# Performance work log

Hardware: AMD Instinct MI355X
Metric: run time of the kernel (lower is better)

## Reference

```python
import jax, jax.numpy as jnp
import numpy as np

N = 50000
IN_F = 512
HID = 64
HEADS = 4
CLASSES = 6
E = 800000
NEG_SLOPE = 0.2


def setup_inputs() -> dict:
    key = jax.random.key(0)
    ks = jax.random.split(key, 12)
    s = 1.0 / np.sqrt(IN_F)
    s2 = 1.0 / np.sqrt(HID * HEADS)
    return {
        "x": jax.random.normal(ks[0], (N, IN_F), dtype=jnp.float32),
        "edge_index": jax.random.randint(ks[1], (2, E), 0, N, dtype=jnp.int32),
        "W1": jax.random.normal(ks[2], (IN_F, HEADS * HID), dtype=jnp.float32) * s,
        "a_src1": jax.random.normal(ks[3], (HEADS, HID), dtype=jnp.float32) * s,
        "a_dst1": jax.random.normal(ks[4], (HEADS, HID), dtype=jnp.float32) * s,
        "b1": jnp.zeros((HEADS * HID,), dtype=jnp.float32),
        "W2": jax.random.normal(ks[5], (HEADS * HID, CLASSES), dtype=jnp.float32) * s2,
        "a_src2": jax.random.normal(ks[6], (1, CLASSES), dtype=jnp.float32) * s2,
        "a_dst2": jax.random.normal(ks[7], (1, CLASSES), dtype=jnp.float32) * s2,
        "b2": jnp.zeros((CLASSES,), dtype=jnp.float32),
    }


def gat_conv(x, src, dst, W, a_src, a_dst, bias, heads, ch):
    # x: [N, F] -> h: [N, H, C]
    n = x.shape[0]
    h = (x @ W).reshape(n, heads, ch)
    # per-node attention halves: [N, H]
    e_src = jnp.einsum('nhc,hc->nh', h, a_src)
    e_dst = jnp.einsum('nhc,hc->nh', h, a_dst)
    # per-edge logits with leaky relu: [E', H]
    logits = jax.nn.leaky_relu(e_src[src] + e_dst[dst], NEG_SLOPE)
    # segment softmax over incoming edges of each dst node
    m = jax.ops.segment_max(logits, dst, num_segments=n)  # [N, H]
    p = jnp.exp(logits - m[dst])
    denom = jax.ops.segment_sum(p, dst, num_segments=n)   # [N, H] (>0: self loops)
    alpha = p / denom[dst]                                 # [E', H]
    # weighted scatter-aggregate: [N, H, C]
    out = jax.ops.segment_sum(alpha[:, :, None] * h[src], dst, num_segments=n)
    return out.reshape(n, heads * ch) + bias


def reference(x, edge_index, W1, a_src1, a_dst1, b1, W2, a_src2, a_dst2, b2):
    n = x.shape[0]
    loops = jnp.arange(n, dtype=edge_index.dtype)
    src = jnp.concatenate([edge_index[0], loops])  # PyG add_self_loops
    dst = jnp.concatenate([edge_index[1], loops])
    h = gat_conv(x, src, dst, W1, a_src1, a_dst1, b1, HEADS, HID)
    h = jax.nn.elu(h)
    out = gat_conv(h, src, dst, W2, a_src2, a_dst2, b2, 1, CLASSES)
    return jax.nn.log_softmax(out, axis=1)
```

## Files before the change

### kernel.cpp

```cpp
#include <hip/hip_runtime.h>

#define HEADS 4
#define HID 64
#define CH1 256
#define CLS 6
#define H2S 8
#define NSLOPE 0.2f

typedef short bf16x8 __attribute__((ext_vector_type(8)));
typedef float f32x4 __attribute__((ext_vector_type(4)));

__device__ __forceinline__ float leaky(float x) {
  return (x >= 0.f) ? x : NSLOPE * x;
}

__device__ __forceinline__ ushort f2bf(float f) {
  unsigned u = __float_as_uint(f);
  unsigned r = (u + 0x7FFFu + ((u >> 16) & 1u)) >> 16;
  return (ushort)r;
}

__device__ __forceinline__ float bf2f(ushort u) {
  return __uint_as_float((unsigned)u << 16);
}

__global__ void k_count_cvt(const int* __restrict__ ei, int E, int Etot,
                            int* __restrict__ cnt, int eb,
                            const float* __restrict__ W1, ushort* __restrict__ w1t) {
  int b = blockIdx.x;
  if (b < eb) {
    int e = b * 256 + threadIdx.x;
    if (e >= Etot) return;
    int d = (e < E) ? ei[E + e] : e - E;
    atomicAdd(&cnt[d], 1);
  } else {
    int t = (b - eb) * 256 + threadIdx.x;
    if (t >= 512 * 256) return;
    int k = t >> 8, c = t & 255;
    w1t[c * 512 + k] = f2bf(W1[t]);
  }
}

__global__ __launch_bounds__(256) void k_gemm1_mfma(
    const float* __restrict__ x,
    const ushort* __restrict__ w1t,
    const float* __restrict__ a_src, const float* __restrict__ a_dst,
    ushort* __restrict__ h1b, float* __restrict__ es, float* __restrict__ ed,
    int M) {
  __shared__ ushort ldsA[2][2048];
  int t = threadIdx.x;
  int wid = t >> 6, lane = t & 63;
  int brow = blockIdx.x * 64;

  int rA = t >> 2, qA = t & 3, lsA = qA ^ (rA & 3);
  int rowA = brow + rA; if (rowA >= M) rowA = M - 1;
  const float* srcA = x + (size_t)rowA * 512 + lsA * 8;
  int dAw = t * 8;

  int l15 = lane & 15, g = lane >> 4;
  int sw = ((g ^ (lane & 3)) << 3);
  int aoff[4];
#pragma unroll
  for (int m = 0; m < 4; ++m) aoff[m] = (m * 16 + l15) * 32 + sw;

  const ushort* bp[4];
#pragma unroll
  for (int n = 0; n < 4; ++n)
    bp[n] = w1t + (size_t)(wid * 64 + n * 16 + l15) * 512 + g * 8;

  f32x4 acc[4][4] = {};
  f32x4 aLo, aHi;

#define LOADA(kt) do { \
    aLo = *(const f32x4*)(srcA + (kt) * 32); \
    aHi = *(const f32x4*)(srcA + (kt) * 32 + 4); \
  } while (0)

#define WRITEA(buf) do { \
    union { unsigned u[4]; bf16x8 b; } cv; \
    asm("v_cvt_pk_bf16_f32 %0, %1, %2" : "=v"(cv.u[0]) : "v"(aLo[0]), "v"(aLo[1])); \
    asm("v_cvt_pk_bf16_f32 %0, %1, %2" : "=v"(cv.u[1]) : "v"(aLo[2]), "v"(aLo[3])); \
    asm("v_cvt_pk_bf16_f32 %0, %1, %2" : "=v"(cv.u[2]) : "v"(aHi[0]), "v"(aHi[1])); \
    asm("v_cvt_pk_bf16_f32 %0, %1, %2" : "=v"(cv.u[3]) : "v"(aHi[2]), "v"(aHi[3])); \
    *(bf16x8*)&ldsA[buf][dAw] = cv.b; \
  } while (0)

  bf16x8 bv[2][4];
#pragma unroll
  for (int n = 0; n < 4; ++n) bv[0][n] = *(const bf16x8*)bp[n];
  LOADA(0);
  WRITEA(0);
  __syncthreads();

#pragma unroll
  for (int kt = 0; kt < 16; ++kt) {
    const int cur = kt & 1;
    if (kt < 15) {
      LOADA(kt + 1);
#pragma unroll
      for (int n = 0; n < 4; ++n)
        bv[(kt + 1) & 1][n] = *(const bf16x8*)(bp[n] + (kt + 1) * 32);
    }
    bf16x8 av[4];
#pragma unroll
    for (int m = 0; m < 4; ++m) av[m] = *(const bf16x8*)&ldsA[cur][aoff[m]];
#pragma unroll
    for (int m = 0; m < 4; ++m)
#pragma unroll
      for (int n = 0; n < 4; ++n)
        acc[m][n] = __builtin_amdgcn_mfma_f32_16x16x32_bf16(av[m], bv[cur][n], acc[m][n], 0, 0, 0);
    if (kt < 15) WRITEA(cur ^ 1);
    __syncthreads();
  }
#undef LOADA
#undef WRITEA

  float as4[4], ad4[4];
#pragma unroll
  for (int n = 0; n < 4; ++n) {
    int c = wid * 64 + n * 16 + l15;
    as4[n] = a_src[c];
    ad4[n] = a_dst[c];
  }
  int rbase = g * 4;
#pragma unroll
  for (int m = 0; m < 4; ++m) {
#pragma unroll
    for (int r = 0; r < 4; ++r) {
      int grow = brow + m * 16 + rbase + r;
      bool ok = grow < M;
      float ps = 0.f, pd = 0.f;
#pragma unroll
      for (int n = 0; n < 4; ++n) {
        float v = acc[m][n][r];
        ps += v * as4[n];
        pd += v * ad4[n];
        if (ok) h1b[(size_t)grow * CH1 + wid * 64 + n * 16 + l15] = f2bf(v);
      }
#pragma unroll
      for (int o = 1; o < 16; o <<= 1) {
        ps += __shfl_xor(ps, o);
        pd += __shfl_xor(pd, o);
      }
      if (l15 == 0 && ok) {
        es[grow * HEADS + wid] = ps;
        ed[grow * HEADS + wid] = pd;
      }
    }
  }
}

__global__ __launch_bounds__(256) void k_scan1(int* __restrict__ deg,
    int* __restrict__ rowptr, int* __restrict__ bsum, int n) {
  int i = blockIdx.x * 256 + threadIdx.x;
  int v = (i < n) ? deg[i] : 0;
  if (i < n) deg[i] = 0;
  int lane = threadIdx.x & 63, wave = threadIdx.x >> 6;
  int incl = v;
#pragma unroll
  for (int o = 1; o < 64; o <<= 1) {
    int u = __shfl_up(incl, o);
    if (lane >= o) incl += u;
  }
  __shared__ int ws4[4];
  if (lane == 63) ws4[wave] = incl;
  __syncthreads();
  if (threadIdx.x == 0) {
    int run = 0;
    for (int w = 0; w < 4; ++w) { int x = ws4[w]; ws4[w] = run; run += x; }
    bsum[blockIdx.x] = run;
  }
  __syncthreads();
  if (i < n) rowptr[i] = incl - v + ws4[wave];
}

__global__ __launch_bounds__(256) void k_scan3(int* __restrict__ rowptr,
    const int* __restrict__ bsum, int n, int Etot, int nb) {
  int t = threadIdx.x;
  int b = blockIdx.x;
  int v = (t < b && t < nb) ? bsum[t] : 0;
  int lane = t & 63, wave = t >> 6;
#pragma unroll
  for (int o = 32; o; o >>= 1) v += __shfl_xor(v, o);
  __shared__ int ws4[4];
  if (lane == 0) ws4[wave] = v;
  __syncthreads();
  int base = ws4[0] + ws4[1] + ws4[2] + ws4[3];
  int i = b * 256 + t;
  if (i < n) rowptr[i] += base;
  if (i == 0) rowptr[n] = Etot;
}

__global__ void k_scatter(const int* __restrict__ ei, int E, int Etot,
    const int* __restrict__ rowptr, int* __restrict__ cursor,
    int* __restrict__ esrc) {
  int e = blockIdx.x * blockDim.x + threadIdx.x;
  if (e >= Etot) return;
  int s, d;
  if (e < E) { s = ei[e]; d = ei[E + e]; } else { s = d = e - E; }
  int pos = rowptr[d] + atomicAdd(&cursor[d], 1);
  esrc[pos] = s;
}

__global__ __launch_bounds__(256) void k_agg1_csr(const int* __restrict__ rowptr,
    const int* __restrict__ esrc, const float* __restrict__ es,
    const float* __restrict__ ed, const ushort* __restrict__ h1b,
    const float* __restrict__ b1, const float* __restrict__ W2,
    const float* __restrict__ a_src2, const float* __restrict__ a_dst2,
    float* __restrict__ h2, float* __restrict__ es2, float* __restrict__ ed2,
    int Nn) {
  __shared__ int   spi[4][64];
  __shared__ float spp[4][64 * 4];
  int wid = threadIdx.x >> 6, lane = threadIdx.x & 63;
  int ch = lane * 4;
  float w2s[4][CLS];
#pragma unroll
  for (int c = 0; c < 4; ++c)
#pragma unroll
    for (int j = 0; j < CLS; ++j)
      w2s[c][j] = W2[(ch + c) * CLS + j];

  int d = blockIdx.x * 4 + wid;
  if (d >= Nn) return;
  int beg = rowptr[d], end = rowptr[d + 1];
  float4 edv = *(const float4*)&ed[d * 4];
  int myhead = lane >> 4;
  const char* hcb = (const char*)h1b + (size_t)ch * 2;

  float4 acc = make_float4(0.f, 0.f, 0.f, 0.f);
  float4 den4 = make_float4(0.f, 0.f, 0.f, 0.f);
  const float* pp = &spp[wid][0];
  for (int c0 = beg; c0 < end; c0 += 64) {
    int i = c0 + lane;
    int s = 0;
    float4 p = make_float4(0.f, 0.f, 0.f, 0.f);
    if (i < end) {
      s = esrc[i];
      float4 e4 = *(const float4*)&es[s * 4];
      p.x = __expf(leaky(e4.x + edv.x));
      p.y = __expf(leaky(e4.y + edv.y));
      p.z = __expf(leaky(e4.z + edv.z));
      p.w = __expf(leaky(e4.w + edv.w));
    }
    den4.x += p.x; den4.y += p.y; den4.z += p.z; den4.w += p.w;
    spi[wid][lane] = s << 9;
    *(float4*)&spp[wid][lane * 4] = p;
    int cl = min(64, end - c0);
    int j = 0;
    for (; j + 3 < cl; j += 4) {
      int o0 = spi[wid][j],     o1 = spi[wid][j + 1];
      int o2 = spi[wid][j + 2], o3 = spi[wid][j + 3];
      float p0 = pp[j * 4 + myhead],       p1 = pp[(j + 1) * 4 + myhead];
      float p2 = pp[(j + 2) * 4 + myhead], p3 = pp[(j + 3) * 4 + myhead];
      ushort4 v0 = *(const ushort4*)(hcb + o0);
      ushort4 v1 = *(const ushort4*)(hcb + o1);
      ushort4 v2 = *(const ushort4*)(hcb + o2);
      ushort4 v3 = *(const ushort4*)(hcb + o3);
      acc.x += p0 * bf2f(v0.x) + p1 * bf2f(v1.x) + p2 * bf2f(v2.x) + p3 * bf2f(v3.x);
      acc.y += p0 * bf2f(v0.y) + p1 * bf2f(v1.y) + p2 * bf2f(v2.y) + p3 * bf2f(v3.y);
      acc.z += p0 * bf2f(v0.z) + p1 * bf2f(v1.z) + p2 * bf2f(v2.z) + p3 * bf2f(v3.z);
      acc.w += p0 * bf2f(v0.w) + p1 * bf2f(v1.w) + p2 * bf2f(v2.w) + p3 * bf2f(v3.w);
    }
    for (; j < cl; ++j) {
      int oj = spi[wid][j];
      float pj = pp[j * 4 + myhead];
      ushort4 v = *(const ushort4*)(hcb + oj);
      acc.x += pj * bf2f(v.x);
      acc.y += pj * bf2f(v.y);
      acc.z += pj * bf2f(v.z);
      acc.w += pj * bf2f(v.w);
    }
  }
#pragma unroll
  for (int o = 32; o; o >>= 1) {
    den4.x += __shfl_xor(den4.x, o);
    den4.y += __shfl_xor(den4.y, o);
    den4.z += __shfl_xor(den4.z, o);
    den4.w += __shfl_xor(den4.w, o);
  }
  float den = (myhead == 0) ? den4.x : (myhead == 1) ? den4.y
            : (myhead == 2) ? den4.z : den4.w;
  float4 b4 = *(const float4*)&b1[ch];
  float4 r;
  r.x = acc.x / den + b4.x; r.x = (r.x > 0.f) ? r.x : expm1f(r.x);
  r.y = acc.y / den + b4.y; r.y = (r.y > 0.f) ? r.y : expm1f(r.y);
  r.z = acc.z / den + b4.z; r.z = (r.z > 0.f) ? r.z : expm1f(r.z);
  r.w = acc.w / den + b4.w; r.w = (r.w > 0.f) ? r.w : expm1f(r.w);

  float q0 = r.x * w2s[0][0] + r.y * w2s[1][0] + r.z * w2s[2][0] + r.w * w2s[3][0];
  float q1 = r.x * w2s[0][1] + r.y * w2s[1][1] + r.z * w2s[2][1] + r.w * w2s[3][1];
  float q2 = r.x * w2s[0][2] + r.y * w2s[1][2] + r.z * w2s[2][2] + r.w * w2s[3][2];
  float q3 = r.x * w2s[0][3] + r.y * w2s[1][3] + r.z * w2s[2][3] + r.w * w2s[3][3];
  float q4 = r.x * w2s[0][4] + r.y * w2s[1][4] + r.z * w2s[2][4] + r.w * w2s[3][4];
  float q5 = r.x * w2s[0][5] + r.y * w2s[1][5] + r.z * w2s[2][5] + r.w * w2s[3][5];
#pragma unroll
  for (int o = 32; o; o >>= 1) {
    q0 += __shfl_xor(q0, o); q1 += __shfl_xor(q1, o); q2 += __shfl_xor(q2, o);
    q3 += __shfl_xor(q3, o); q4 += __shfl_xor(q4, o); q5 += __shfl_xor(q5, o);
  }
  if (lane == 0) {
    float* h2r = &h2[(size_t)d * H2S];
    h2r[0] = q0; h2r[1] = q1; h2r[2] = q2; h2r[3] = q3; h2r[4] = q4; h2r[5] = q5;
    es2[d] = q0 * a_src2[0] + q1 * a_src2[1] + q2 * a_src2[2]
           + q3 * a_src2[3] + q4 * a_src2[4] + q5 * a_src2[5];
    ed2[d] = q0 * a_dst2[0] + q1 * a_dst2[1] + q2 * a_dst2[2]
           + q3 * a_dst2[3] + q4 * a_dst2[4] + q5 * a_dst2[5];
  }
}

__global__ __launch_bounds__(256) void k_l2(const int* __restrict__ rowptr,
    const int* __restrict__ esrc, const float* __restrict__ es2,
    const float* __restrict__ ed2, const float* __restrict__ h2,
    const float* __restrict__ b2, float* __restrict__ out, int Nn) {
  int t = threadIdx.x;
  int grp = t >> 3, sl = t & 7;
  int n = blockIdx.x * 32 + grp;
  if (n >= Nn) return;
  int beg = rowptr[n], end = rowptr[n + 1];
  float edv = ed2[n];
  float den = 0.f, a0 = 0.f, a1 = 0.f, a2 = 0.f, a3 = 0.f, a4 = 0.f, a5 = 0.f;
  for (int i = beg + sl; i < end; i += 8) {
    int s = esrc[i];
    float p = __expf(leaky(es2[s] + edv));
    den += p;
    const float* hr = &h2[(size_t)s * H2S];
    float4 v0 = *(const float4*)hr;
    float2 v1 = *(const float2*)(hr + 4);
    a0 += p * v0.x; a1 += p * v0.y; a2 += p * v0.z;
    a3 += p * v0.w; a4 += p * v1.x; a5 += p * v1.y;
  }
#pragma unroll
  for (int o = 1; o < 8; o <<= 1) {
    den += __shfl_xor(den, o);
    a0 += __shfl_xor(a0, o); a1 += __shfl_xor(a1, o); a2 += __shfl_xor(a2, o);
    a3 += __shfl_xor(a3, o); a4 += __shfl_xor(a4, o); a5 += __shfl_xor(a5, o);
  }
  if (sl == 0) {
    float v[CLS];
    v[0] = a0 / den + b2[0]; v[1] = a1 / den + b2[1]; v[2] = a2 / den + b2[2];
    v[3] = a3 / den + b2[3]; v[4] = a4 / den + b2[4]; v[5] = a5 / den + b2[5];
    float mx = -1e30f;
#pragma unroll
    for (int j = 0; j < CLS; ++j) mx = fmaxf(mx, v[j]);
    float sum = 0.f;
#pragma unroll
    for (int j = 0; j < CLS; ++j) sum += __expf(v[j] - mx);
    float l = mx + logf(sum);
#pragma unroll
    for (int j = 0; j < CLS; ++j) out[n * CLS + j] = v[j] - l;
  }
}

extern "C" void kernel_launch(void* const* d_in, const int* in_sizes, int n_in,
                              void* d_out, int out_size, void* d_ws, size_t ws_size,
                              hipStream_t stream) {
  const float* x      = (const float*)d_in[0];
  const int*   ei     = (const int*)d_in[1];
  const float* W1     = (const float*)d_in[2];
  const float* a_src1 = (const float*)d_in[3];
  const float* a_dst1 = (const float*)d_in[4];
  const float* b1     = (const float*)d_in[5];
  const float* W2     = (const float*)d_in[6];
  const float* a_src2 = (const float*)d_in[7];
  const float* a_dst2 = (const float*)d_in[8];
  const float* b2     = (const float*)d_in[9];
  float* out = (float*)d_out;

  const int IN_F = 512;
  int N = in_sizes[0] / IN_F;
  int E = in_sizes[1] / 2;
  int Etot = E + N;

  float* ws = (float*)d_ws;
  size_t off = 0;
  ushort* h1b = (ushort*)(ws + off); off += (size_t)N * CH1;
  float* es1  = ws + off; off += (size_t)N * HEADS;
  float* ed1  = ws + off; off += (size_t)N * HEADS;
  float* h2   = ws + off; off += (size_t)N * H2S;
  float* es2  = ws + off; off += (size_t)N;
  float* ed2  = ws + off; off += (size_t)N;
  int* rowptr = (int*)(ws + off); off += (size_t)N + 1;
  int* cursor = (int*)(ws + off); off += (size_t)N;
  int* bsum   = (int*)(ws + off); off += 256;
  int* esrc   = (int*)(ws + off); off += (size_t)Etot;
  ushort* w1t = (ushort*)(ws + off); off += (512 * 256 * 2 + 3) / 4;

  int nb = (N + 255) / 256;
  int eb = (Etot + 255) / 256;

  hipMemsetAsync(cursor, 0, (size_t)N * 4, stream);
  k_count_cvt<<<eb + 512, 256, 0, stream>>>(ei, E, Etot, cursor, eb, W1, w1t);
  k_scan1<<<nb, 256, 0, stream>>>(cursor, rowptr, bsum, N);
  k_scan3<<<nb, 256, 0, stream>>>(rowptr, bsum, N, Etot, nb);
  k_scatter<<<eb, 256, 0, stream>>>(ei, E, Etot, rowptr, cursor, esrc);

  k_gemm1_mfma<<<(N + 63) / 64, 256, 0, stream>>>(x, w1t, a_src1, a_dst1,
                                                  h1b, es1, ed1, N);
  k_agg1_csr<<<(N + 3) / 4, 256, 0, stream>>>(rowptr, esrc, es1, ed1, h1b, b1,
                                              W2, a_src2, a_dst2, h2, es2, ed2, N);

  k_l2<<<(N + 31) / 32, 256, 0, stream>>>(rowptr, esrc, es2, ed2, h2, b2, out, N);
}
```

Baseline: 241.1 us.

## Load GEMM1 A operand directly from global into registers, drop LDS staging

The first-layer GEMM no longer stages the converted x tile through double-buffered shared memory with block barriers. Each wave now loads its own A fragments straight from global memory, converts them to bf16 in registers, and prefetches the next k-step. Launch bounds also request two blocks per CU. This removes the LDS writes, reads and __syncthreads, but each of the four waves now reads the same x rows separately, so global/L2 traffic for A is four times higher and register pressure grows.

```diff
diff --git a/kernel.cpp b/kernel.cpp
--- a/kernel.cpp
+++ b/kernel.cpp
@@ -41,79 +41,70 @@
   }
 }
 
-__global__ __launch_bounds__(256) void k_gemm1_mfma(
+__global__ __launch_bounds__(256, 2) void k_gemm1_mfma(
     const float* __restrict__ x,
     const ushort* __restrict__ w1t,
     const float* __restrict__ a_src, const float* __restrict__ a_dst,
     ushort* __restrict__ h1b, float* __restrict__ es, float* __restrict__ ed,
     int M) {
-  __shared__ ushort ldsA[2][2048];
   int t = threadIdx.x;
   int wid = t >> 6, lane = t & 63;
   int brow = blockIdx.x * 64;
-
-  int rA = t >> 2, qA = t & 3, lsA = qA ^ (rA & 3);
-  int rowA = brow + rA; if (rowA >= M) rowA = M - 1;
-  const float* srcA = x + (size_t)rowA * 512 + lsA * 8;
-  int dAw = t * 8;
-
   int l15 = lane & 15, g = lane >> 4;
-  int sw = ((g ^ (lane & 3)) << 3);
-  int aoff[4];
-#pragma unroll
-  for (int m = 0; m < 4; ++m) aoff[m] = (m * 16 + l15) * 32 + sw;
-
+
+  const float* ap[4];
+#pragma unroll
+  for (int m = 0; m < 4; ++m) {
+    int r = brow + m * 16 + l15; if (r >= M) r = M - 1;
+    ap[m] = x + (size_t)r * 512 + g * 8;
+  }
   const ushort* bp[4];
 #pragma unroll
   for (int n = 0; n < 4; ++n)
     bp[n] = w1t + (size_t)(wid * 64 + n * 16 + l15) * 512 + g * 8;
 
   f32x4 acc[4][4] = {};
-  f32x4 aLo, aHi;
-
-#define LOADA(kt) do { \
-    aLo = *(const f32x4*)(srcA + (kt) * 32); \
-    aHi = *(const f32x4*)(srcA + (kt) * 32 + 4); \
-  } while (0)
-
-#define WRITEA(buf) do { \
-    union { unsigned u[4]; bf16x8 b; } cv; \
-    asm("v_cvt_pk_bf16_f32 %0, %1, %2" : "=v"(cv.u[0]) : "v"(aLo[0]), "v"(aLo[1])); \
-    asm("v_cvt_pk_bf16_f32 %0, %1, %2" : "=v"(cv.u[1]) : "v"(aLo[2]), "v"(aLo[3])); \
-    asm("v_cvt_pk_bf16_f32 %0, %1, %2" : "=v"(cv.u[2]) : "v"(aHi[0]), "v"(aHi[1])); \
-    asm("v_cvt_pk_bf16_f32 %0, %1, %2" : "=v"(cv.u[3]) : "v"(aHi[2]), "v"(aHi[3])); \
-    *(bf16x8*)&ldsA[buf][dAw] = cv.b; \
-  } while (0)
-
-  bf16x8 bv[2][4];
-#pragma unroll
-  for (int n = 0; n < 4; ++n) bv[0][n] = *(const bf16x8*)bp[n];
-  LOADA(0);
-  WRITEA(0);
-  __syncthreads();
+
+  f32x4 nLo[4], nHi[4];
+  bf16x8 nB[4];
+#pragma unroll
+  for (int m = 0; m < 4; ++m) {
+    nLo[m] = *(const f32x4*)(ap[m]);
+    nHi[m] = *(const f32x4*)(ap[m] + 4);
+  }
+#pragma unroll
+  for (int n = 0; n < 4; ++n) nB[n] = *(const bf16x8*)bp[n];
 
 #pragma unroll
   for (int kt = 0; kt < 16; ++kt) {
-    const int cur = kt & 1;
+    bf16x8 av[4], bv[4];
+#pragma unroll
+    for (int m = 0; m < 4; ++m) {
+      union { unsigned u[4]; bf16x8 b; } cv;
+      asm("v_cvt_pk_bf16_f32 %0, %1, %2" : "=v"(cv.u[0]) : "v"(nLo[m][0]), "v"(nLo[m][1]));
+      asm("v_cvt_pk_bf16_f32 %0, %1, %2" : "=v"(cv.u[1]) : "v"(nLo[m][2]), "v"(nLo[m][3]));
+      asm("v_cvt_pk_bf16_f32 %0, %1, %2" : "=v"(cv.u[2]) : "v"(nHi[m][0]), "v"(nHi[m][1]));
+      asm("v_cvt_pk_bf16_f32 %0, %1, %2" : "=v"(cv.u[3]) : "v"(nHi[m][2]), "v"(nHi[m][3]));
+      av[m] = cv.b;
+    }
+#pragma unroll
+    for (int n = 0; n < 4; ++n) bv[n] = nB[n];
     if (kt < 15) {
-      LOADA(kt + 1);
+#pragma unroll
+      for (int m = 0; m < 4; ++m) {
+        nLo[m] = *(const f32x4*)(ap[m] + (kt + 1) * 32);
+        nHi[m] = *(const f32x4*)(ap[m] + (kt + 1) * 32 + 4);
+      }
 #pragma unroll
       for (int n = 0; n < 4; ++n)
-        bv[(kt + 1) & 1][n] = *(const bf16x8*)(bp[n] + (kt + 1) * 32);
-    }
-    bf16x8 av[4];
-#pragma unroll
-    for (int m = 0; m < 4; ++m) av[m] = *(const bf16x8*)&ldsA[cur][aoff[m]];
+        nB[n] = *(const bf16x8*)(bp[n] + (kt + 1) * 32);
+    }
 #pragma unroll
     for (int m = 0; m < 4; ++m)
 #pragma unroll
       for (int n = 0; n < 4; ++n)
-        acc[m][n] = __builtin_amdgcn_mfma_f32_16x16x32_bf16(av[m], bv[cur][n], acc[m][n], 0, 0, 0);
-    if (kt < 15) WRITEA(cur ^ 1);
-    __syncthreads();
-  }
-#undef LOADA
-#undef WRITEA
+        acc[m][n] = __builtin_amdgcn_mfma_f32_16x16x32_bf16(av[m], bv[n], acc[m][n], 0, 0, 0);
+  }
 
   float as4[4], ad4[4];
 #pragma unroll
```

New measurement: 293.2 us. +21.6%, slower.

## Split GEMM1 columns across two blocks per row tile to raise occupancy

Applied to the files above, without the earlier changes.

Each 64-row tile of the first-layer GEMM now gets two blocks, one per 128-column half. Every wave holds 4x2 accumulators instead of 4x4, and launch bounds request 4 blocks per CU. Because each head now spans two waves, the attention dot products are reduced through shared memory before being written out. The aim is more blocks in flight and lower register pressure, at the cost of converting and loading the x tile twice from global memory.

```diff
diff --git a/kernel.cpp b/kernel.cpp
--- a/kernel.cpp
+++ b/kernel.cpp
@@ -41,34 +41,37 @@
   }
 }
 
-__global__ __launch_bounds__(256) void k_gemm1_mfma(
+__global__ __launch_bounds__(256, 4) void k_gemm1_mfma(
     const float* __restrict__ x,
     const ushort* __restrict__ w1t,
     const float* __restrict__ a_src, const float* __restrict__ a_dst,
     ushort* __restrict__ h1b, float* __restrict__ es, float* __restrict__ ed,
     int M) {
   __shared__ ushort ldsA[2][2048];
+  __shared__ float pes[4][64], ped[4][64];
   int t = threadIdx.x;
   int wid = t >> 6, lane = t & 63;
-  int brow = blockIdx.x * 64;
+  int brow = (blockIdx.x >> 1) * 64;
+  int bcol = (blockIdx.x & 1) * 128;
+  int l15 = lane & 15, g = lane >> 4;
 
   int rA = t >> 2, qA = t & 3, lsA = qA ^ (rA & 3);
   int rowA = brow + rA; if (rowA >= M) rowA = M - 1;
   const float* srcA = x + (size_t)rowA * 512 + lsA * 8;
   int dAw = t * 8;
 
-  int l15 = lane & 15, g = lane >> 4;
   int sw = ((g ^ (lane & 3)) << 3);
   int aoff[4];
 #pragma unroll
   for (int m = 0; m < 4; ++m) aoff[m] = (m * 16 + l15) * 32 + sw;
 
-  const ushort* bp[4];
-#pragma unroll
-  for (int n = 0; n < 4; ++n)
-    bp[n] = w1t + (size_t)(wid * 64 + n * 16 + l15) * 512 + g * 8;
-
-  f32x4 acc[4][4] = {};
+  int colb = bcol + wid * 32;
+  const ushort* bp[2];
+#pragma unroll
+  for (int n = 0; n < 2; ++n)
+    bp[n] = w1t + (size_t)(colb + n * 16 + l15) * 512 + g * 8;
+
+  f32x4 acc[4][2] = {};
   f32x4 aLo, aHi;
 
 #define LOADA(kt) do { \
@@ -85,9 +88,9 @@
     *(bf16x8*)&ldsA[buf][dAw] = cv.b; \
   } while (0)
 
-  bf16x8 bv[2][4];
-#pragma unroll
-  for (int n = 0; n < 4; ++n) bv[0][n] = *(const bf16x8*)bp[n];
+  bf16x8 bv[2][2];
+#pragma unroll
+  for (int n = 0; n < 2; ++n) bv[0][n] = *(const bf16x8*)bp[n];
   LOADA(0);
   WRITEA(0);
   __syncthreads();
@@ -98,7 +101,7 @@
     if (kt < 15) {
       LOADA(kt + 1);
 #pragma unroll
-      for (int n = 0; n < 4; ++n)
+      for (int n = 0; n < 2; ++n)
         bv[(kt + 1) & 1][n] = *(const bf16x8*)(bp[n] + (kt + 1) * 32);
     }
     bf16x8 av[4];
@@ -107,7 +110,7 @@
 #pragma unroll
     for (int m = 0; m < 4; ++m)
 #pragma unroll
-      for (int n = 0; n < 4; ++n)
+      for (int n = 0; n < 2; ++n)
         acc[m][n] = __builtin_amdgcn_mfma_f32_16x16x32_bf16(av[m], bv[cur][n], acc[m][n], 0, 0, 0);
     if (kt < 15) WRITEA(cur ^ 1);
     __syncthreads();
@@ -115,37 +118,48 @@
 #undef LOADA
 #undef WRITEA
 
-  float as4[4], ad4[4];
-#pragma unroll
-  for (int n = 0; n < 4; ++n) {
-    int c = wid * 64 + n * 16 + l15;
-    as4[n] = a_src[c];
-    ad4[n] = a_dst[c];
+  float as2[2], ad2[2];
+#pragma unroll
+  for (int n = 0; n < 2; ++n) {
+    int c = colb + n * 16 + l15;
+    as2[n] = a_src[c];
+    ad2[n] = a_dst[c];
   }
   int rbase = g * 4;
 #pragma unroll
   for (int m = 0; m < 4; ++m) {
 #pragma unroll
     for (int r = 0; r < 4; ++r) {
-      int grow = brow + m * 16 + rbase + r;
+      int ri = m * 16 + rbase + r;
+      int grow = brow + ri;
       bool ok = grow < M;
       float ps = 0.f, pd = 0.f;
 #pragma unroll
-      for (int n = 0; n < 4; ++n) {
+      for (int n = 0; n < 2; ++n) {
         float v = acc[m][n][r];
-        ps += v * as4[n];
-        pd += v * ad4[n];
-        if (ok) h1b[(size_t)grow * CH1 + wid * 64 + n * 16 + l15] = f2bf(v);
+        ps += v * as2[n];
+        pd += v * ad2[n];
+        if (ok) h1b[(size_t)grow * CH1 + colb + n * 16 + l15] = f2bf(v);
       }
 #pragma unroll
       for (int o = 1; o < 16; o <<= 1) {
         ps += __shfl_xor(ps, o);
         pd += __shfl_xor(pd, o);
       }
-      if (l15 == 0 && ok) {
-        es[grow * HEADS + wid] = ps;
-        ed[grow * HEADS + wid] = pd;
+      if (l15 == 0) {
+        pes[wid][ri] = ps;
+        ped[wid][ri] = pd;
       }
+    }
+  }
+  __syncthreads();
+  if (t < 128) {
+    int ri = t & 63, hp = t >> 6;
+    int grow = brow + ri;
+    if (grow < M) {
+      int head = (bcol >> 6) + hp;
+      es[grow * HEADS + head] = pes[2 * hp][ri] + pes[2 * hp + 1][ri];
+      ed[grow * HEADS + head] = ped[2 * hp][ri] + ped[2 * hp + 1][ri];
     }
   }
 }
@@ -394,8 +408,8 @@
   k_scan3<<<nb, 256, 0, stream>>>(rowptr, bsum, N, Etot, nb);
   k_scatter<<<eb, 256, 0, stream>>>(ei, E, Etot, rowptr, cursor, esrc);
 
-  k_gemm1_mfma<<<(N + 63) / 64, 256, 0, stream>>>(x, w1t, a_src1, a_dst1,
-                                                  h1b, es1, ed1, N);
+  k_gemm1_mfma<<<((N + 63) / 64) * 2, 256, 0, stream>>>(x, w1t, a_src1, a_dst1,
+                                                        h1b, es1, ed1, N);
   k_agg1_csr<<<(N + 3) / 4, 256, 0, stream>>>(rowptr, esrc, es1, ed1, h1b, b1,
                                               W2, a_src2, a_dst2, h2, es2, ed2, N);
 
```

After: 247.1 us. 1.02x slower.

## Pre-convert x to bf16, stage GEMM tiles via global_load_lds, fuse scatter

Applied to the files above, without the earlier changes.

Converts x to bf16 in a separate pass fused into the count/W1-convert launch. The layer-1 GEMM then stages both A and B tiles into LDS with direct global-to-LDS 16-byte loads instead of register loads plus in-register conversion. The CSR scatter kernel is merged into the GEMM launch as extra blocks, so its work can overlap with the GEMM. The intent is to cut register pressure and load latency in the GEMM and save a launch, at the cost of extra global traffic: x is read, written as bf16, then read again.

```diff
diff --git a/kernel.cpp b/kernel.cpp
--- a/kernel.cpp
+++ b/kernel.cpp
@@ -24,96 +24,112 @@
   return __uint_as_float((unsigned)u << 16);
 }
 
-__global__ void k_count_cvt(const int* __restrict__ ei, int E, int Etot,
-                            int* __restrict__ cnt, int eb,
-                            const float* __restrict__ W1, ushort* __restrict__ w1t) {
+__device__ __forceinline__ void gload16(const void* g, void* l) {
+  __builtin_amdgcn_global_load_lds((const __attribute__((address_space(1))) void*)g,
+                                   (__attribute__((address_space(3))) void*)l, 16, 0, 0);
+}
+
+__global__ void k_count_cvt_x(const int* __restrict__ ei, int E, int Etot,
+                              int* __restrict__ cnt, int eb,
+                              const float* __restrict__ W1, ushort* __restrict__ w1t,
+                              const float* __restrict__ x, ushort* __restrict__ xb,
+                              long nx) {
   int b = blockIdx.x;
   if (b < eb) {
     int e = b * 256 + threadIdx.x;
     if (e >= Etot) return;
     int d = (e < E) ? ei[E + e] : e - E;
     atomicAdd(&cnt[d], 1);
-  } else {
+  } else if (b < eb + 512) {
     int t = (b - eb) * 256 + threadIdx.x;
     if (t >= 512 * 256) return;
     int k = t >> 8, c = t & 255;
     w1t[c * 512 + k] = f2bf(W1[t]);
-  }
-}
-
-__global__ __launch_bounds__(256) void k_gemm1_mfma(
-    const float* __restrict__ x,
+  } else {
+    long i = ((long)(b - eb - 512) * 256 + threadIdx.x) * 4;
+    long stride = 2048L * 1024;
+    for (; i + 3 < nx; i += stride) {
+      float4 v = *(const float4*)&x[i];
+      ushort4 o;
+      o.x = f2bf(v.x); o.y = f2bf(v.y); o.z = f2bf(v.z); o.w = f2bf(v.w);
+      *(ushort4*)&xb[i] = o;
+    }
+  }
+}
+
+__global__ __launch_bounds__(256) void k_gemm1_scatter(
+    const ushort* __restrict__ xb,
     const ushort* __restrict__ w1t,
     const float* __restrict__ a_src, const float* __restrict__ a_dst,
     ushort* __restrict__ h1b, float* __restrict__ es, float* __restrict__ ed,
-    int M) {
-  __shared__ ushort ldsA[2][2048];
+    int M, int G1,
+    const int* __restrict__ ei, int E, int Etot,
+    const int* __restrict__ rowptr, int* __restrict__ cursor,
+    int* __restrict__ esrc) {
+  __shared__ ushort lds[2][10240];
   int t = threadIdx.x;
+
+  if (blockIdx.x >= G1) {
+    int e = (blockIdx.x - G1) * 256 + t;
+    if (e >= Etot) return;
+    int s, d;
+    if (e < E) { s = ei[e]; d = ei[E + e]; } else { s = d = e - E; }
+    int pos = rowptr[d] + atomicAdd(&cursor[d], 1);
+    esrc[pos] = s;
+    return;
+  }
+
   int wid = t >> 6, lane = t & 63;
   int brow = blockIdx.x * 64;
 
-  int rA = t >> 2, qA = t & 3, lsA = qA ^ (rA & 3);
+  int rA = t >> 2;
+  int sA = (t & 3) ^ (rA & 3);
   int rowA = brow + rA; if (rowA >= M) rowA = M - 1;
-  const float* srcA = x + (size_t)rowA * 512 + lsA * 8;
-  int dAw = t * 8;
+  const ushort* srcA  = xb  + (size_t)rowA * 512 + sA * 8;
+  int cB = t >> 2;
+  int sB = (t & 3) ^ (cB & 3);
+  const ushort* srcB0 = w1t + (size_t)cB * 512 + sB * 8;
+  int dA = t * 8;
+  int dB = 2048 + t * 8;
 
   int l15 = lane & 15, g = lane >> 4;
   int sw = ((g ^ (lane & 3)) << 3);
-  int aoff[4];
+  int aoff[4], boff[4];
 #pragma unroll
   for (int m = 0; m < 4; ++m) aoff[m] = (m * 16 + l15) * 32 + sw;
-
-  const ushort* bp[4];
-#pragma unroll
-  for (int n = 0; n < 4; ++n)
-    bp[n] = w1t + (size_t)(wid * 64 + n * 16 + l15) * 512 + g * 8;
+#pragma unroll
+  for (int n = 0; n < 4; ++n) boff[n] = 2048 + (wid * 64 + n * 16 + l15) * 32 + sw;
 
   f32x4 acc[4][4] = {};
-  f32x4 aLo, aHi;
-
-#define LOADA(kt) do { \
-    aLo = *(const f32x4*)(srcA + (kt) * 32); \
-    aHi = *(const f32x4*)(srcA + (kt) * 32 + 4); \
+
+#define STAGE(buf, koff) do { \
+    gload16(srcA + (koff),              &lds[buf][dA]); \
+    gload16(srcB0 + (koff),             &lds[buf][dB]); \
+    gload16(srcB0 +  64 * 512 + (koff), &lds[buf][dB + 2048]); \
+    gload16(srcB0 + 128 * 512 + (koff), &lds[buf][dB + 4096]); \
+    gload16(srcB0 + 192 * 512 + (koff), &lds[buf][dB + 6144]); \
   } while (0)
 
-#define WRITEA(buf) do { \
-    union { unsigned u[4]; bf16x8 b; } cv; \
-    asm("v_cvt_pk_bf16_f32 %0, %1, %2" : "=v"(cv.u[0]) : "v"(aLo[0]), "v"(aLo[1])); \
-    asm("v_cvt_pk_bf16_f32 %0, %1, %2" : "=v"(cv.u[1]) : "v"(aLo[2]), "v"(aLo[3])); \
-    asm("v_cvt_pk_bf16_f32 %0, %1, %2" : "=v"(cv.u[2]) : "v"(aHi[0]), "v"(aHi[1])); \
-    asm("v_cvt_pk_bf16_f32 %0, %1, %2" : "=v"(cv.u[3]) : "v"(aHi[2]), "v"(aHi[3])); \
-    *(bf16x8*)&ldsA[buf][dAw] = cv.b; \
-  } while (0)
-
-  bf16x8 bv[2][4];
-#pragma unroll
-  for (int n = 0; n < 4; ++n) bv[0][n] = *(const bf16x8*)bp[n];
-  LOADA(0);
-  WRITEA(0);
+  STAGE(0, 0);
   __syncthreads();
-
-#pragma unroll
+  int cur = 0;
   for (int kt = 0; kt < 16; ++kt) {
-    const int cur = kt & 1;
-    if (kt < 15) {
-      LOADA(kt + 1);
+    if (kt < 15) STAGE(cur ^ 1, (kt + 1) * 32);
+    const ushort* L = lds[cur];
+    bf16x8 av[4], bv[4];
+#pragma unroll
+    for (int m = 0; m < 4; ++m) av[m] = *(const bf16x8*)&L[aoff[m]];
+#pragma unroll
+    for (int n = 0; n < 4; ++n) bv[n] = *(const bf16x8*)&L[boff[n]];
+#pragma unroll
+    for (int m = 0; m < 4; ++m)
 #pragma unroll
       for (int n = 0; n < 4; ++n)
-        bv[(kt + 1) & 1][n] = *(const bf16x8*)(bp[n] + (kt + 1) * 32);
-    }
-    bf16x8 av[4];
-#pragma unroll
-    for (int m = 0; m < 4; ++m) av[m] = *(const bf16x8*)&ldsA[cur][aoff[m]];
-#pragma unroll
-    for (int m = 0; m < 4; ++m)
-#pragma unroll
-      for (int n = 0; n < 4; ++n)
-        acc[m][n] = __builtin_amdgcn_mfma_f32_16x16x32_bf16(av[m], bv[cur][n], acc[m][n], 0, 0, 0);
-    if (kt < 15) WRITEA(cur ^ 1);
+        acc[m][n] = __builtin_amdgcn_mfma_f32_16x16x32_bf16(av[m], bv[n], acc[m][n], 0, 0, 0);
     __syncthreads();
-  }
-#undef LOADA
-#undef WRITEA
+    cur ^= 1;
+  }
+#undef STAGE
 
   float as4[4], ad4[4];
 #pragma unroll
@@ -189,17 +205,6 @@
   int i = b * 256 + t;
   if (i < n) rowptr[i] += base;
   if (i == 0) rowptr[n] = Etot;
-}
-
-__global__ void k_scatter(const int* __restrict__ ei, int E, int Etot,
-    const int* __restrict__ rowptr, int* __restrict__ cursor,
-    int* __restrict__ esrc) {
-  int e = blockIdx.x * blockDim.x + threadIdx.x;
-  if (e >= Etot) return;
-  int s, d;
-  if (e < E) { s = ei[e]; d = ei[E + e]; } else { s = d = e - E; }
-  int pos = rowptr[d] + atomicAdd(&cursor[d], 1);
-  esrc[pos] = s;
 }
 
 __global__ __launch_bounds__(256) void k_agg1_csr(const int* __restrict__ rowptr,
@@ -373,7 +378,8 @@
 
   float* ws = (float*)d_ws;
   size_t off = 0;
-  ushort* h1b = (ushort*)(ws + off); off += (size_t)N * CH1;
+  ushort* xb  = (ushort*)(ws + off); off += (size_t)N * 256;
+  ushort* h1b = (ushort*)(ws + off); off += (size_t)N * 128;
   float* es1  = ws + off; off += (size_t)N * HEADS;
   float* ed1  = ws + off; off += (size_t)N * HEADS;
   float* h2   = ws + off; off += (size_t)N * H2S;
@@ -387,17 +393,19 @@
 
   int nb = (N + 255) / 256;
   int eb = (Etot + 255) / 256;
+  int G1 = (N + 63) / 64;
 
   hipMemsetAsync(cursor, 0, (size_t)N * 4, stream);
-  k_count_cvt<<<eb + 512, 256, 0, stream>>>(ei, E, Etot, cursor, eb, W1, w1t);
+  k_count_cvt_x<<<eb + 512 + 2048, 256, 0, stream>>>(ei, E, Etot, cursor, eb,
+                                                     W1, w1t, x, xb, (long)N * IN_F);
   k_scan1<<<nb, 256, 0, stream>>>(cursor, rowptr, bsum, N);
   k_scan3<<<nb, 256, 0, stream>>>(rowptr, bsum, N, Etot, nb);
-  k_scatter<<<eb, 256, 0, stream>>>(ei, E, Etot, rowptr, cursor, esrc);
-
-  k_gemm1_mfma<<<(N + 63) / 64, 256, 0, stream>>>(x, w1t, a_src1, a_dst1,
-                                                  h1b, es1, ed1, N);
+
+  k_gemm1_scatter<<<G1 + eb, 256, 0, stream>>>(xb, w1t, a_src1, a_dst1,
+                                               h1b, es1, ed1, N, G1,
+                                               ei, E, Etot, rowptr, cursor, esrc);
+
   k_agg1_csr<<<(N + 3) / 4, 256, 0, stream>>>(rowptr, esrc, es1, ed1, h1b, b1,
                                               W2, a_src2, a_dst2, h2, es2, ed2, N);
-
   k_l2<<<(N + 31) / 32, 256, 0, stream>>>(rowptr, esrc, es2, ed2, h2, b2, out, N);
 }
```

Measured after the change: 248.6 us. 3.1% more time.
